# Kernel tuning notes

Hardware: AMD Instinct MI355X
Metric: run time of the kernel (lower is better)

## Reference

```python
import jax, jax.numpy as jnp
import numpy as np

L = 4        # num_layers
D = 1024     # transformer_dim
H = 16       # num_heads
HD = D // H  # head_dim
M = 4096     # mlp_dim
S = 1024     # seq_len
B = 2        # batch
WIN = 2      # temporal_window (one-sided)
EPS = 1e-5   # LayerNorm eps (torch default)


def setup_inputs() -> dict:
    key = jax.random.key(0)
    ks = jax.random.split(key, 16)
    def rn(k, shape, s=0.02):
        return jax.random.normal(k, shape, dtype=jnp.float32) * s
    return {
        "x": jax.random.normal(ks[0], (B, S, D), dtype=jnp.float32),
        # intra-frame MHA params (stacked over layers)
        "w_in1": rn(ks[1], (L, 3 * D, D)), "b_in1": jnp.zeros((L, 3 * D), jnp.float32),
        "w_out1": rn(ks[2], (L, D, D)),    "b_out1": jnp.zeros((L, D), jnp.float32),
        "ln1_g": jnp.ones((L, D), jnp.float32), "ln1_b": jnp.zeros((L, D), jnp.float32),
        # inter-frame (banded) MHA params
        "w_in2": rn(ks[3], (L, 3 * D, D)), "b_in2": jnp.zeros((L, 3 * D), jnp.float32),
        "w_out2": rn(ks[4], (L, D, D)),    "b_out2": jnp.zeros((L, D), jnp.float32),
        "ln2_g": jnp.ones((L, D), jnp.float32), "ln2_b": jnp.zeros((L, D), jnp.float32),
        # FFN params
        "ffn_w1": rn(ks[5], (L, M, D)), "ffn_b1": jnp.zeros((L, M), jnp.float32),
        "ffn_w2": rn(ks[6], (L, D, M)), "ffn_b2": jnp.zeros((L, D), jnp.float32),
        # final norm
        "lnf_g": jnp.ones((D,), jnp.float32), "lnf_b": jnp.zeros((D,), jnp.float32),
    }


def _layernorm(x, g, b):
    mu = jnp.mean(x, axis=-1, keepdims=True)
    var = jnp.mean(jnp.square(x - mu), axis=-1, keepdims=True)
    return (x - mu) * jax.lax.rsqrt(var + EPS) * g + b


def _mha(x, w_in, b_in, w_out, b_out, band):
    # x: [B,S,D]; w_in: [3D,D] packed qkv (torch in_proj layout)
    Bx, Sx, Dx = x.shape
    qkv = x @ w_in.T + b_in                      # [B,S,3D]
    q, k, v = jnp.split(qkv, 3, axis=-1)
    def to_heads(t):
        return t.reshape(Bx, Sx, H, HD).transpose(0, 2, 1, 3)  # [B,H,S,hd]
    q, k, v = to_heads(q), to_heads(k), to_heads(v)
    scores = jnp.einsum('bhsd,bhtd->bhst', q, k) / jnp.sqrt(jnp.float32(HD))
    if band is not None:
        scores = jnp.where(band, scores, -jnp.inf)  # additive -inf band mask
    attn = jax.nn.softmax(scores, axis=-1)
    out = jnp.einsum('bhst,bhtd->bhsd', attn, v)
    out = out.transpose(0, 2, 1, 3).reshape(Bx, Sx, Dx)
    return out @ w_out.T + b_out


def reference(x, w_in1, b_in1, w_out1, b_out1, ln1_g, ln1_b,
              w_in2, b_in2, w_out2, b_out2, ln2_g, ln2_b,
              ffn_w1, ffn_b1, ffn_w2, ffn_b2, lnf_g, lnf_b):
    idx = jnp.arange(S)
    band = jnp.abs(idx[:, None] - idx[None, :]) <= WIN  # [S,S] bool, True=attend
    for l in range(L):
        # intra-frame full MHA + residual + LN
        x_intra = _mha(x, w_in1[l], b_in1[l], w_out1[l], b_out1[l], None)
        x = _layernorm(x + x_intra, ln1_g[l], ln1_b[l])
        # inter-frame banded MHA + residual + LN
        x_inter = _mha(x, w_in2[l], b_in2[l], w_out2[l], b_out2[l], band)
        attended = _layernorm(x + x_inter, ln2_g[l], ln2_b[l])
        # FFN applied to attended; residual from attended (dropout_p=0)
        h = jax.nn.gelu(attended @ ffn_w1[l].T + ffn_b1[l], approximate=False)
        x = attended + (h @ ffn_w2[l].T + ffn_b2[l])
    return _layernorm(x, lnf_g, lnf_b)
```

## Files before the change

kernel.cpp:

```cpp
#include <hip/hip_runtime.h>
#include <math.h>

#define SEQ    1024
#define DIM    1024
#define NH     16
#define HDIM   64
#define MLP    4096
#define NLAYER 4
#define BATCH  2
#define NTOK   (BATCH * SEQ)
#define LN_EPS 1e-5f

typedef unsigned short ushortx;
typedef __attribute__((ext_vector_type(8))) short bf16x8;
typedef __attribute__((ext_vector_type(8))) unsigned short u16x8;
typedef __attribute__((ext_vector_type(4))) float f32x4;

__device__ __forceinline__ float gelu_exact(float x) {
    return 0.5f * x * (1.0f + erff(x * 0.70710678118654752f));
}
__device__ __forceinline__ unsigned int pack2bf(float a, float b) {
    union { float f; unsigned int u; } va, vb;
    va.f = a; vb.f = b;
    unsigned int ua = va.u + 0x7fffu + ((va.u >> 16) & 1u);
    unsigned int ub = vb.u + 0x7fffu + ((vb.u >> 16) & 1u);
    return (ua >> 16) | (ub & 0xffff0000u);
}
__device__ __forceinline__ ushortx bf16lo(float a) {
    return (ushortx)(pack2bf(a, 0.f) & 0xffffu);
}
__device__ __forceinline__ float bf2f(ushortx u) {
    union { unsigned int i; float f; } v; v.i = ((unsigned int)u) << 16; return v.f;
}

__global__ __launch_bounds__(256)
void cvt_w(const float* __restrict__ s0, const float* __restrict__ s1,
           const float* __restrict__ s2, const float* __restrict__ s3,
           const float* __restrict__ s4, const float* __restrict__ s5,
           ushortx* __restrict__ dst)
{
    const size_t total = 4194304;
    for (size_t g = (size_t)blockIdx.x * 256 + threadIdx.x; g < total;
         g += (size_t)gridDim.x * 256) {
        const float* src; size_t base;
        if      (g <  786432) { src = s0; base = 0; }
        else if (g < 1048576) { src = s1; base =  786432; }
        else if (g < 1835008) { src = s2; base = 1048576; }
        else if (g < 2097152) { src = s3; base = 1835008; }
        else if (g < 3145728) { src = s4; base = 2097152; }
        else                  { src = s5; base = 3145728; }
        float4 f = *(const float4*)(src + (g - base) * 4);
        ushort4 o = { bf16lo(f.x), bf16lo(f.y), bf16lo(f.z), bf16lo(f.w) };
        *(ushort4*)(dst + g * 4) = o;
    }
}

__global__ __launch_bounds__(256)
void init_x(const float* __restrict__ x0, float* __restrict__ xb,
            ushortx* __restrict__ xbf)
{
    const size_t i = (size_t)blockIdx.x * 256 + threadIdx.x;
    const float v = x0[i];
    xb[i] = v;
    xbf[i] = bf16lo(v);
}

template<int BM, int BN, int MODE>
__global__ __launch_bounds__(256)
void gemm_bf(const ushortx* __restrict__ A, const ushortx* __restrict__ W,
             const float* __restrict__ bias, void* __restrict__ Cout,
             void* __restrict__ Vout, int K, int N, int kChunk)
{
    constexpr int MT = BM / 32, NT = BN / 32;
    constexpr int AI = BM / 32, WI = BN / 32;
    __shared__ ushortx As[BM][72];
    __shared__ ushortx Ws[BN][72];
    const int t = threadIdx.x;
    const int wave = t >> 6, lane = t & 63, quad = lane >> 4, l16 = lane & 15;
    const int wm = (wave >> 1) * (BM / 2);
    const int wn = (wave & 1) * (BN / 2);
    const int rowBase = blockIdx.y * BM, colBase = blockIdx.x * BN;
    const int kBase = blockIdx.z * kChunk;

    f32x4 acc[MT][NT];
    #pragma unroll
    for (int mt = 0; mt < MT; ++mt)
        #pragma unroll
        for (int nt = 0; nt < NT; ++nt) acc[mt][nt] = (f32x4){0.f, 0.f, 0.f, 0.f};

    u16x8 aR[AI], wR[WI];
    #pragma unroll
    for (int i = 0; i < AI; ++i) {
        const int c = t + 256 * i, r = c >> 3, c8 = (c & 7) * 8;
        aR[i] = *(const u16x8*)(A + (size_t)(rowBase + r) * K + kBase + c8);
    }
    #pragma unroll
    for (int i = 0; i < WI; ++i) {
        const int c = t + 256 * i, r = c >> 3, c8 = (c & 7) * 8;
        wR[i] = *(const u16x8*)(W + (size_t)(colBase + r) * K + kBase + c8);
    }
    const int nIt = kChunk / 64;
    for (int kt = 0; kt < nIt; ++kt) {
        __syncthreads();
        #pragma unroll
        for (int i = 0; i < AI; ++i) {
            const int c = t + 256 * i;
            *(u16x8*)&As[c >> 3][(c & 7) * 8] = aR[i];
        }
        #pragma unroll
        for (int i = 0; i < WI; ++i) {
            const int c = t + 256 * i;
            *(u16x8*)&Ws[c >> 3][(c & 7) * 8] = wR[i];
        }
        __syncthreads();
        if (kt + 1 < nIt) {
            const int k0 = kBase + (kt + 1) * 64;
            #pragma unroll
            for (int i = 0; i < AI; ++i) {
                const int c = t + 256 * i, r = c >> 3, c8 = (c & 7) * 8;
                aR[i] = *(const u16x8*)(A + (size_t)(rowBase + r) * K + k0 + c8);
            }
            #pragma unroll
            for (int i = 0; i < WI; ++i) {
                const int c = t + 256 * i, r = c >> 3, c8 = (c & 7) * 8;
                wR[i] = *(const u16x8*)(W + (size_t)(colBase + r) * K + k0 + c8);
            }
        }
        #pragma unroll
        for (int kk = 0; kk < 2; ++kk) {
            bf16x8 af[MT], bfv[NT];
            #pragma unroll
            for (int mt = 0; mt < MT; ++mt)
                af[mt] = *(const bf16x8*)&As[wm + mt * 16 + l16][kk * 32 + quad * 8];
            #pragma unroll
            for (int nt = 0; nt < NT; ++nt)
                bfv[nt] = *(const bf16x8*)&Ws[wn + nt * 16 + l16][kk * 32 + quad * 8];
            #pragma unroll
            for (int mt = 0; mt < MT; ++mt)
                #pragma unroll
                for (int nt = 0; nt < NT; ++nt)
                    acc[mt][nt] = __builtin_amdgcn_mfma_f32_16x16x32_bf16(
                        af[mt], bfv[nt], acc[mt][nt], 0, 0, 0);
        }
    }
    #pragma unroll
    for (int mt = 0; mt < MT; ++mt) {
        #pragma unroll
        for (int nt = 0; nt < NT; ++nt) {
            const int colTile = colBase + wn + nt * 16;
            const int col = colTile + l16;
            const float bv = (blockIdx.z == 0) ? bias[col] : 0.f;
            const int rbase = rowBase + wm + mt * 16 + quad * 4;
            if (MODE == 0) {
                float* C = (blockIdx.z == 0)
                    ? (float*)Cout
                    : (float*)Vout + (size_t)(blockIdx.z - 1) *
                          ((size_t)gridDim.y * BM) * N;
                #pragma unroll
                for (int r = 0; r < 4; ++r)
                    C[(size_t)(rbase + r) * N + col] = acc[mt][nt][r] + bv;
            } else if (MODE == 1) {
                ushortx* C = (ushortx*)Cout;
                #pragma unroll
                for (int r = 0; r < 4; ++r)
                    C[(size_t)(rbase + r) * N + col] = bf16lo(gelu_exact(acc[mt][nt][r] + bv));
            } else if (MODE == 3) {
                ushortx* C = (ushortx*)Cout;
                #pragma unroll
                for (int r = 0; r < 4; ++r)
                    C[(size_t)(rbase + r) * (3 * DIM) + col] = bf16lo(acc[mt][nt][r] + bv);
            } else {
                if (colTile < 2 * DIM) {
                    ushortx* C = (ushortx*)Cout;
                    #pragma unroll
                    for (int r = 0; r < 4; ++r)
                        C[(size_t)(rbase + r) * (2 * DIM) + col] = bf16lo(acc[mt][nt][r] + bv);
                } else {
                    ushortx* vt = (ushortx*)Vout;
                    const int cb = col - 2 * DIM;
                    const int hh = cb >> 6, dd = cb & 63;
                    const int bb = rbase >> 10, s0 = rbase & 1023;
                    ushort4 pk = { bf16lo(acc[mt][nt][0] + bv), bf16lo(acc[mt][nt][1] + bv),
                                   bf16lo(acc[mt][nt][2] + bv), bf16lo(acc[mt][nt][3] + bv) };
                    *(ushort4*)&vt[((size_t)((bb * 16 + hh) * 64 + dd) << 10) + s0] = pk;
                }
            }
        }
    }
}

__global__ __launch_bounds__(256)
void attn_full(const ushortx* __restrict__ qk, const ushortx* __restrict__ vt,
               ushortx* __restrict__ outb)
{
    __shared__ ushortx Qs[64][72];
    __shared__ ushortx Ks[2][64][72];
    __shared__ ushortx VT[2][64][72];
    __shared__ ushortx Ps[4][16][72];

    const int blk = blockIdx.x;
    const int q0 = (blk & 15) * 64;
    const int h  = (blk >> 4) & 15;
    const int b  = blk >> 8;
    const int t  = threadIdx.x;
    const int w = t >> 6, lane = t & 63;
    const int quad = lane >> 4, l16 = lane & 15;

    const int c0 = t,       r0 = c0 >> 3, c80 = (c0 & 7) * 8;
    const int c1 = t + 256, r1 = c1 >> 3, c81 = (c1 & 7) * 8;

    *(u16x8*)&Qs[r0][c80] =
        *(const u16x8*)(qk + (size_t)(b * SEQ + q0 + r0) * (2 * DIM) + h * HDIM + c80);
    *(u16x8*)&Qs[r1][c81] =
        *(const u16x8*)(qk + (size_t)(b * SEQ + q0 + r1) * (2 * DIM) + h * HDIM + c81);

    const ushortx* kbase = qk + (size_t)(b * SEQ) * (2 * DIM) + DIM + h * HDIM;
    const ushortx* vbase = vt + ((size_t)((b * 16 + h) * 64) << 10);

    u16x8 kR0 = *(const u16x8*)(kbase + (size_t)r0 * (2 * DIM) + c80);
    u16x8 kR1 = *(const u16x8*)(kbase + (size_t)r1 * (2 * DIM) + c81);
    u16x8 vR0 = *(const u16x8*)(vbase + ((size_t)r0 << 10) + c80);
    u16x8 vR1 = *(const u16x8*)(vbase + ((size_t)r1 << 10) + c81);

    __syncthreads();
    bf16x8 aq0 = *(const bf16x8*)&Qs[w * 16 + l16][quad * 8];
    bf16x8 aq1 = *(const bf16x8*)&Qs[w * 16 + l16][32 + quad * 8];

    float m_r[4] = {-1e30f, -1e30f, -1e30f, -1e30f};
    float l_r[4] = {0.f, 0.f, 0.f, 0.f};
    f32x4 Oa[4];
    #pragma unroll
    for (int nt = 0; nt < 4; ++nt) Oa[nt] = (f32x4){0.f, 0.f, 0.f, 0.f};

    int buf = 0;
    for (int kt = 0; kt < SEQ / 64; ++kt) {
        *(u16x8*)&Ks[buf][r0][c80] = kR0;
        *(u16x8*)&Ks[buf][r1][c81] = kR1;
        *(u16x8*)&VT[buf][r0][c80] = vR0;
        *(u16x8*)&VT[buf][r1][c81] = vR1;
        __syncthreads();

        if (kt + 1 < SEQ / 64) {
            const int k0 = (kt + 1) * 64;
            kR0 = *(const u16x8*)(kbase + (size_t)(k0 + r0) * (2 * DIM) + c80);
            kR1 = *(const u16x8*)(kbase + (size_t)(k0 + r1) * (2 * DIM) + c81);
            vR0 = *(const u16x8*)(vbase + ((size_t)r0 << 10) + k0 + c80);
            vR1 = *(const u16x8*)(vbase + ((size_t)r1 << 10) + k0 + c81);
        }

        f32x4 s[4];
        #pragma unroll
        for (int nt = 0; nt < 4; ++nt) {
            bf16x8 bk0 = *(const bf16x8*)&Ks[buf][nt * 16 + l16][quad * 8];
            bf16x8 bk1 = *(const bf16x8*)&Ks[buf][nt * 16 + l16][32 + quad * 8];
            s[nt] = __builtin_amdgcn_mfma_f32_16x16x32_bf16(aq0, bk0,
                        (f32x4){0.f, 0.f, 0.f, 0.f}, 0, 0, 0);
            s[nt] = __builtin_amdgcn_mfma_f32_16x16x32_bf16(aq1, bk1, s[nt], 0, 0, 0);
        }
        float tm[4], alpha[4];
        #pragma unroll
        for (int r = 0; r < 4; ++r) {
            float v = fmaxf(fmaxf(s[0][r], s[1][r]), fmaxf(s[2][r], s[3][r])) * 0.125f;
            #pragma unroll
            for (int off = 1; off < 16; off <<= 1) v = fmaxf(v, __shfl_xor(v, off));
            tm[r] = v;
        }
        #pragma unroll
        for (int r = 0; r < 4; ++r) {
            const float mn = fmaxf(m_r[r], tm[r]);
            alpha[r] = __expf(m_r[r] - mn);
            m_r[r] = mn;
        }
        float rs[4] = {0.f, 0.f, 0.f, 0.f};
        #pragma unroll
        for (int nt = 0; nt < 4; ++nt) {
            #pragma unroll
            for (int r = 0; r < 4; ++r) {
                const float p = __expf(s[nt][r] * 0.125f - m_r[r]);
                rs[r] += p;
                Ps[w][quad * 4 + r][nt * 16 + l16] = bf16lo(p);
            }
        }
        #pragma unroll
        for (int r = 0; r < 4; ++r) {
            float v = rs[r];
            #pragma unroll
            for (int off = 1; off < 16; off <<= 1) v += __shfl_xor(v, off);
            l_r[r] = l_r[r] * alpha[r] + v;
            #pragma unroll
            for (int nt = 0; nt < 4; ++nt) Oa[nt][r] *= alpha[r];
        }
        bf16x8 pa0 = *(const bf16x8*)&Ps[w][l16][quad * 8];
        bf16x8 pa1 = *(const bf16x8*)&Ps[w][l16][32 + quad * 8];
        #pragma unroll
        for (int nt = 0; nt < 4; ++nt) {
            bf16x8 bv0 = *(const bf16x8*)&VT[buf][nt * 16 + l16][quad * 8];
            bf16x8 bv1 = *(const bf16x8*)&VT[buf][nt * 16 + l16][32 + quad * 8];
            Oa[nt] = __builtin_amdgcn_mfma_f32_16x16x32_bf16(pa0, bv0, Oa[nt], 0, 0, 0);
            Oa[nt] = __builtin_amdgcn_mfma_f32_16x16x32_bf16(pa1, bv1, Oa[nt], 0, 0, 0);
        }
        buf ^= 1;
    }
    float inv[4];
    #pragma unroll
    for (int r = 0; r < 4; ++r) inv[r] = 1.f / l_r[r];
    #pragma unroll
    for (int r = 0; r < 4; ++r) {
        const size_t row = (size_t)(b * SEQ + q0 + w * 16 + quad * 4 + r);
        #pragma unroll
        for (int nt = 0; nt < 4; ++nt)
            outb[row * DIM + h * HDIM + nt * 16 + l16] = bf16lo(Oa[nt][r] * inv[r]);
    }
}

__global__ __launch_bounds__(256)
void attn_band(const ushortx* __restrict__ qkv, ushortx* __restrict__ outb)
{
    const int blk = blockIdx.x;
    const int chunk = blk & (SEQ / 32 - 1);
    const int h = (blk >> 5) & (NH - 1);
    const int b = blk >> 9;
    const int tid = threadIdx.x;
    const int s = chunk * 32 + (tid >> 3);
    const int oct = tid & 7;
    const size_t base = (size_t)(b * SEQ) * (3 * DIM) + h * HDIM + oct * 8;

    float qf[8];
    {
        u16x8 qv = *(const u16x8*)(qkv + base + (size_t)s * (3 * DIM));
        #pragma unroll
        for (int j = 0; j < 8; ++j) qf[j] = bf2f((ushortx)qv[j]);
    }

    float sc[5];
    #pragma unroll
    for (int o = 0; o < 5; ++o) {
        const int tt = s - 2 + o;
        const bool valid = ((unsigned)tt < SEQ);
        float d = 0.f;
        if (valid) {
            u16x8 kv = *(const u16x8*)(qkv + base + (size_t)tt * (3 * DIM) + DIM);
            #pragma unroll
            for (int j = 0; j < 8; ++j) d += qf[j] * bf2f((ushortx)kv[j]);
        }
        d += __shfl_xor(d, 1);
        d += __shfl_xor(d, 2);
        d += __shfl_xor(d, 4);
        sc[o] = valid ? d * 0.125f : -1e30f;
    }
    const float m = fmaxf(fmaxf(fmaxf(sc[0], sc[1]), fmaxf(sc[2], sc[3])), sc[4]);
    float p[5], sum = 0.f;
    #pragma unroll
    for (int o = 0; o < 5; ++o) { p[o] = __expf(sc[o] - m); sum += p[o]; }
    const float inv = 1.f / sum;

    float acc[8] = {0.f, 0.f, 0.f, 0.f, 0.f, 0.f, 0.f, 0.f};
    #pragma unroll
    for (int o = 0; o < 5; ++o) {
        const int tt = s - 2 + o;
        if ((unsigned)tt < SEQ) {
            u16x8 vv = *(const u16x8*)(qkv + base + (size_t)tt * (3 * DIM) + 2 * DIM);
            #pragma unroll
            for (int j = 0; j < 8; ++j) acc[j] += p[o] * bf2f((ushortx)vv[j]);
        }
    }
    unsigned int o01 = pack2bf(acc[0] * inv, acc[1] * inv);
    unsigned int o23 = pack2bf(acc[2] * inv, acc[3] * inv);
    unsigned int o45 = pack2bf(acc[4] * inv, acc[5] * inv);
    unsigned int o67 = pack2bf(acc[6] * inv, acc[7] * inv);
    uint4 st = { o01, o23, o45, o67 };
    *(uint4*)(outb + (size_t)(b * SEQ + s) * DIM + h * HDIM + oct * 8) = st;
}

__global__ __launch_bounds__(256)
void add_ln(const float* __restrict__ x, const float* __restrict__ y,
            const float* __restrict__ g, const float* __restrict__ be,
            float* __restrict__ outf, ushortx* __restrict__ outb, int hasY)
{
    __shared__ float row[DIM];
    __shared__ float red[256];
    const int n = blockIdx.x;
    const int tid = threadIdx.x;
    float lsum = 0.f;
    for (int i = tid; i < DIM; i += 256) {
        float v = x[(size_t)n * DIM + i];
        if (hasY) v += y[(size_t)n * DIM + i];
        row[i] = v;
        lsum += v;
    }
    red[tid] = lsum;
    __syncthreads();
    for (int ofs = 128; ofs > 0; ofs >>= 1) {
        if (tid < ofs) red[tid] += red[tid + ofs];
        __syncthreads();
    }
    const float mu = red[0] * (1.f / DIM);
    __syncthreads();
    float lvar = 0.f;
    for (int i = tid; i < DIM; i += 256) {
        const float d = row[i] - mu;
        lvar += d * d;
    }
    red[tid] = lvar;
    __syncthreads();
    for (int ofs = 128; ofs > 0; ofs >>= 1) {
        if (tid < ofs) red[tid] += red[tid + ofs];
        __syncthreads();
    }
    const float rstd = rsqrtf(red[0] * (1.f / DIM) + LN_EPS);
    __syncthreads();
    for (int i = tid; i < DIM; i += 256) {
        const float o = (row[i] - mu) * rstd * g[i] + be[i];
        if (outf) outf[(size_t)n * DIM + i] = o;
        if (outb) outb[(size_t)n * DIM + i] = bf16lo(o);
    }
}

__global__ __launch_bounds__(256)
void add_vec(const float* __restrict__ a, const float* __restrict__ b,
             float* __restrict__ outf, ushortx* __restrict__ outb)
{
    const size_t i = (size_t)blockIdx.x * 256 + threadIdx.x;
    const float v = a[i] + b[i];
    outf[i] = v;
    outb[i] = bf16lo(v);
}

__global__ __launch_bounds__(256)
void add_vec4(const float* __restrict__ a, const float* __restrict__ p0,
              const float* __restrict__ p1, const float* __restrict__ p2,
              const float* __restrict__ p3,
              float* __restrict__ outf, ushortx* __restrict__ outb)
{
    const size_t i = (size_t)blockIdx.x * 256 + threadIdx.x;
    const float v = a[i] + ((p0[i] + p1[i]) + (p2[i] + p3[i]));
    outf[i] = v;
    outb[i] = bf16lo(v);
}

extern "C" void kernel_launch(void* const* d_in, const int* in_sizes, int n_in,
                              void* d_out, int out_size, void* d_ws, size_t ws_size,
                              hipStream_t stream)
{
    const float* x0     = (const float*)d_in[0];
    const float* w_in1  = (const float*)d_in[1];
    const float* b_in1  = (const float*)d_in[2];
    const float* w_out1 = (const float*)d_in[3];
    const float* b_out1 = (const float*)d_in[4];
    const float* ln1_g  = (const float*)d_in[5];
    const float* ln1_b  = (const float*)d_in[6];
    const float* w_in2  = (const float*)d_in[7];
    const float* b_in2  = (const float*)d_in[8];
    const float* w_out2 = (const float*)d_in[9];
    const float* b_out2 = (const float*)d_in[10];
    const float* ln2_g  = (const float*)d_in[11];
    const float* ln2_b  = (const float*)d_in[12];
    const float* fw1    = (const float*)d_in[13];
    const float* fb1    = (const float*)d_in[14];
    const float* fw2    = (const float*)d_in[15];
    const float* fb2    = (const float*)d_in[16];
    const float* lnf_g  = (const float*)d_in[17];
    const float* lnf_b  = (const float*)d_in[18];
    float* out = (float*)d_out;

    char* W = (char*)d_ws;
    float*   xb    = (float*)(W);
    float*   t2    = (float*)(W + ((size_t)8  << 20));
    float*   attf  = (float*)(W + ((size_t)16 << 20));
    ushortx* actbf = (ushortx*)(W + ((size_t)24 << 20));
    ushortx* qkb   = (ushortx*)(W + ((size_t)28 << 20));
    ushortx* vtb   = (ushortx*)(W + ((size_t)36 << 20));
    ushortx* hbf   = (ushortx*)(W + ((size_t)28 << 20));
    ushortx* wbf   = (ushortx*)(W + ((size_t)44 << 20));
    float*   pk1   = (float*)(W + ((size_t)44 << 20));

    const size_t OFF_WI1 = 0,        OFF_WO1 = 3145728;
    const size_t OFF_WI2 = 4194304,  OFF_WO2 = 7340032;
    const size_t OFF_W1  = 8388608,  OFF_W2  = 12582912;

    init_x<<<dim3(NTOK * DIM / 256), dim3(256), 0, stream>>>(x0, xb, actbf);

    const dim3 blk(256);
    for (int l = 0; l < NLAYER; ++l) {
        const float* bi1 = b_in1  + (size_t)l * 3 * DIM;
        const float* bo1 = b_out1 + (size_t)l * DIM;
        const float* g1  = ln1_g  + (size_t)l * DIM;
        const float* be1 = ln1_b  + (size_t)l * DIM;
        const float* bi2 = b_in2  + (size_t)l * 3 * DIM;
        const float* bo2 = b_out2 + (size_t)l * DIM;
        const float* g2  = ln2_g  + (size_t)l * DIM;
        const float* be2 = ln2_b  + (size_t)l * DIM;
        const float* b1l = fb1    + (size_t)l * MLP;
        const float* b2l = fb2    + (size_t)l * DIM;

        cvt_w<<<dim3(2048), blk, 0, stream>>>(
            w_in1 + (size_t)l * 3 * DIM * DIM, w_out1 + (size_t)l * DIM * DIM,
            w_in2 + (size_t)l * 3 * DIM * DIM, w_out2 + (size_t)l * DIM * DIM,
            fw1 + (size_t)l * MLP * DIM, fw2 + (size_t)l * DIM * MLP, wbf);

        gemm_bf<128, 128, 2><<<dim3(3 * DIM / 128, NTOK / 128), blk, 0, stream>>>(
            actbf, wbf + OFF_WI1, bi1, qkb, vtb, DIM, 0, DIM);
        attn_full<<<dim3(BATCH * NH * (SEQ / 64)), blk, 0, stream>>>(qkb, vtb, actbf);
        gemm_bf<64, 64, 0><<<dim3(DIM / 64, NTOK / 64), blk, 0, stream>>>(
            actbf, wbf + OFF_WO1, bo1, t2, nullptr, DIM, DIM, DIM);
        add_ln<<<dim3(NTOK), blk, 0, stream>>>(xb, t2, g1, be1, xb, actbf, 1);
        gemm_bf<128, 128, 3><<<dim3(3 * DIM / 128, NTOK / 128), blk, 0, stream>>>(
            actbf, wbf + OFF_WI2, bi2, qkb, nullptr, DIM, 3 * DIM, DIM);
        attn_band<<<dim3(BATCH * NH * (SEQ / 32)), blk, 0, stream>>>(qkb, actbf);
        gemm_bf<64, 64, 0><<<dim3(DIM / 64, NTOK / 64), blk, 0, stream>>>(
            actbf, wbf + OFF_WO2, bo2, t2, nullptr, DIM, DIM, DIM);
        add_ln<<<dim3(NTOK), blk, 0, stream>>>(xb, t2, g2, be2, attf, actbf, 1);
        gemm_bf<128, 128, 1><<<dim3(MLP / 128, NTOK / 128), blk, 0, stream>>>(
            actbf, wbf + OFF_W1, b1l, hbf, nullptr, DIM, MLP, DIM);
        gemm_bf<128, 128, 0><<<dim3(DIM / 128, NTOK / 128, 4), blk, 0, stream>>>(
            hbf, wbf + OFF_W2, b2l, t2, pk1, MLP, DIM, MLP / 4);
        add_vec4<<<dim3(NTOK * DIM / 256), blk, 0, stream>>>(
            attf, t2, pk1, pk1 + (size_t)NTOK * DIM, pk1 + (size_t)2 * NTOK * DIM,
            xb, actbf);
    }
    add_ln<<<dim3(NTOK), blk, 0, stream>>>(xb, nullptr, lnf_g, lnf_b, out, nullptr, 0);
}
```

Baseline: 1.128 ms.

## Load GEMM tiles directly global-to-LDS with XOR-swizzled unpadded layout

```diff
diff --git a/kernel.cpp b/kernel.cpp
--- a/kernel.cpp
+++ b/kernel.cpp
@@ -31,6 +31,11 @@
 }
 __device__ __forceinline__ float bf2f(ushortx u) {
     union { unsigned int i; float f; } v; v.i = ((unsigned int)u) << 16; return v.f;
+}
+__device__ __forceinline__ void gload16(const void* g, void* l) {
+    __builtin_amdgcn_global_load_lds(
+        (const __attribute__((address_space(1))) unsigned int*)g,
+        (__attribute__((address_space(3))) unsigned int*)l, 16, 0, 0);
 }
 
 __global__ __launch_bounds__(256)
@@ -73,8 +78,8 @@
 {
     constexpr int MT = BM / 32, NT = BN / 32;
     constexpr int AI = BM / 32, WI = BN / 32;
-    __shared__ ushortx As[BM][72];
-    __shared__ ushortx Ws[BN][72];
+    __shared__ ushortx As[BM * 64];
+    __shared__ ushortx Ws[BN * 64];
     const int t = threadIdx.x;
     const int wave = t >> 6, lane = t & 63, quad = lane >> 4, l16 = lane & 15;
     const int wm = (wave >> 1) * (BM / 2);
@@ -82,59 +87,53 @@
     const int rowBase = blockIdx.y * BM, colBase = blockIdx.x * BN;
     const int kBase = blockIdx.z * kChunk;
 
+    const int srow = t >> 3, schunk = t & 7;
+    const ushortx* aSrc[AI];
+    const ushortx* wSrc[WI];
+    #pragma unroll
+    for (int i = 0; i < AI; ++i) {
+        const int r = srow + 32 * i;
+        aSrc[i] = A + (size_t)(rowBase + r) * K + kBase + (schunk ^ (r & 7)) * 8;
+    }
+    #pragma unroll
+    for (int i = 0; i < WI; ++i) {
+        const int r = srow + 32 * i;
+        wSrc[i] = W + (size_t)(colBase + r) * K + kBase + (schunk ^ (r & 7)) * 8;
+    }
+    char* asB = (char*)As + wave * 1024;
+    char* wsB = (char*)Ws + wave * 1024;
+
     f32x4 acc[MT][NT];
     #pragma unroll
     for (int mt = 0; mt < MT; ++mt)
         #pragma unroll
         for (int nt = 0; nt < NT; ++nt) acc[mt][nt] = (f32x4){0.f, 0.f, 0.f, 0.f};
 
-    u16x8 aR[AI], wR[WI];
-    #pragma unroll
-    for (int i = 0; i < AI; ++i) {
-        const int c = t + 256 * i, r = c >> 3, c8 = (c & 7) * 8;
-        aR[i] = *(const u16x8*)(A + (size_t)(rowBase + r) * K + kBase + c8);
-    }
-    #pragma unroll
-    for (int i = 0; i < WI; ++i) {
-        const int c = t + 256 * i, r = c >> 3, c8 = (c & 7) * 8;
-        wR[i] = *(const u16x8*)(W + (size_t)(colBase + r) * K + kBase + c8);
-    }
     const int nIt = kChunk / 64;
     for (int kt = 0; kt < nIt; ++kt) {
+        if (kt) __syncthreads();
+        #pragma unroll
+        for (int i = 0; i < AI; ++i)
+            gload16(aSrc[i] + kt * 64, asB + i * 4096);
+        #pragma unroll
+        for (int i = 0; i < WI; ++i)
+            gload16(wSrc[i] + kt * 64, wsB + i * 4096);
         __syncthreads();
-        #pragma unroll
-        for (int i = 0; i < AI; ++i) {
-            const int c = t + 256 * i;
-            *(u16x8*)&As[c >> 3][(c & 7) * 8] = aR[i];
-        }
-        #pragma unroll
-        for (int i = 0; i < WI; ++i) {
-            const int c = t + 256 * i;
-            *(u16x8*)&Ws[c >> 3][(c & 7) * 8] = wR[i];
-        }
-        __syncthreads();
-        if (kt + 1 < nIt) {
-            const int k0 = kBase + (kt + 1) * 64;
-            #pragma unroll
-            for (int i = 0; i < AI; ++i) {
-                const int c = t + 256 * i, r = c >> 3, c8 = (c & 7) * 8;
-                aR[i] = *(const u16x8*)(A + (size_t)(rowBase + r) * K + k0 + c8);
-            }
-            #pragma unroll
-            for (int i = 0; i < WI; ++i) {
-                const int c = t + 256 * i, r = c >> 3, c8 = (c & 7) * 8;
-                wR[i] = *(const u16x8*)(W + (size_t)(colBase + r) * K + k0 + c8);
-            }
-        }
         #pragma unroll
         for (int kk = 0; kk < 2; ++kk) {
             bf16x8 af[MT], bfv[NT];
             #pragma unroll
-            for (int mt = 0; mt < MT; ++mt)
-                af[mt] = *(const bf16x8*)&As[wm + mt * 16 + l16][kk * 32 + quad * 8];
-            #pragma unroll
-            for (int nt = 0; nt < NT; ++nt)
-                bfv[nt] = *(const bf16x8*)&Ws[wn + nt * 16 + l16][kk * 32 + quad * 8];
+            for (int mt = 0; mt < MT; ++mt) {
+                const int r = wm + mt * 16 + l16;
+                af[mt] = *(const bf16x8*)
+                    &As[r * 64 + (((kk * 4 + quad) ^ (r & 7)) * 8)];
+            }
+            #pragma unroll
+            for (int nt = 0; nt < NT; ++nt) {
+                const int r = wn + nt * 16 + l16;
+                bfv[nt] = *(const bf16x8*)
+                    &Ws[r * 64 + (((kk * 4 + quad) ^ (r & 7)) * 8)];
+            }
             #pragma unroll
             for (int mt = 0; mt < MT; ++mt)
                 #pragma unroll
@@ -417,16 +416,6 @@
 }
 
 __global__ __launch_bounds__(256)
-void add_vec(const float* __restrict__ a, const float* __restrict__ b,
-             float* __restrict__ outf, ushortx* __restrict__ outb)
-{
-    const size_t i = (size_t)blockIdx.x * 256 + threadIdx.x;
-    const float v = a[i] + b[i];
-    outf[i] = v;
-    outb[i] = bf16lo(v);
-}
-
-__global__ __launch_bounds__(256)
 void add_vec4(const float* __restrict__ a, const float* __restrict__ p0,
               const float* __restrict__ p1, const float* __restrict__ p2,
               const float* __restrict__ p3,
```

After: 1.098 ms. -2.6%, faster.
